# Performance work log

Hardware: AMD Instinct MI355X
Metric: run time of the kernel (lower is better)

Reference implementation:

```python
import jax, jax.numpy as jnp
import numpy as np

H0, H1, NHID, BATCH = 256, 256, 512, 2048

def setup_inputs() -> dict:
    key = jax.random.key(0)
    k1, k2, k3, k4, k5 = jax.random.split(key, 5)
    initrange = 0.1
    inputs = jax.random.normal(k1, (BATCH, NHID), dtype=jnp.float32)
    labels = jax.random.randint(k2, (BATCH,), 0, H1, dtype=jnp.int32)
    parent_labels = jax.random.randint(k3, (BATCH,), 0, H0, dtype=jnp.int32)
    layer_top_W = jax.random.uniform(k4, (NHID, H0), jnp.float32, -initrange, initrange)
    layer_top_b = jnp.zeros((H0,), jnp.float32)
    layer_bottom_W = jax.random.uniform(k5, (H0, NHID, H1), jnp.float32, -initrange, initrange)
    layer_bottom_b = jnp.zeros((H0, H1), jnp.float32)
    return {"inputs": inputs, "labels": labels, "parent_labels": parent_labels,
            "layer_top_W": layer_top_W, "layer_top_b": layer_top_b,
            "layer_bottom_W": layer_bottom_W, "layer_bottom_b": layer_bottom_b}

def reference(inputs, labels, parent_labels, layer_top_W, layer_top_b,
              layer_bottom_W, layer_bottom_b):
    batch = inputs.shape[0]
    # top-level softmax over coarse classes: [B, H0]
    top_probs = jax.nn.softmax(inputs @ layer_top_W + layer_top_b, axis=1)
    # per-sample gather of expert weight slice [B, NHID, H1] then bmm
    Wb = layer_bottom_W[parent_labels]            # [B, NHID, H1]
    bb = layer_bottom_b[parent_labels]            # [B, H1]
    bottom_logits = jnp.einsum('bd,bdk->bk', inputs, Wb) + bb
    bottom_probs = jax.nn.softmax(bottom_logits, axis=1)
    ar = jnp.arange(batch)
    target_probs = top_probs[ar, parent_labels] * bottom_probs[ar, labels]
    return target_probs
```

## Files before the change

kernel.cpp:

```cpp
#include <hip/hip_runtime.h>

constexpr int BATCH = 2048;
constexpr int NHID  = 512;
constexpr int H0    = 256;
constexpr int H1    = 256;
constexpr int SMAX  = 32;
constexpr int KS    = NHID / 4;

__global__ __launch_bounds__(512, 2) void hs_ksplit(
    const float* __restrict__ x,
    const int*   __restrict__ labels,
    const int*   __restrict__ parents,
    const float* __restrict__ topW,
    const float* __restrict__ topb,
    const float* __restrict__ botW,
    const float* __restrict__ botb,
    float*       __restrict__ out)
{
    const int p  = blockIdx.x;
    const int t  = threadIdx.x;
    const int g  = t >> 6;
    const int l  = t & 63;
    const int kw = g & 3;
    const bool bot = (g < 4);

    __shared__ int list[BATCH];
    __shared__ int wcnt[8];
    __shared__ __align__(16) float  xs[SMAX][NHID];
    __shared__ __align__(16) float4 redB[3][4][64];
    __shared__ __align__(16) float4 redT[3][4][64];
    __shared__ float psm[2][SMAX];

    int running = 0;
    for (int c = 0; c < BATCH; c += 512) {
        const bool match = (parents[c + t] == p);
        const unsigned long long mask = __ballot(match);
        if (l == 0) wcnt[g] = __popcll(mask);
        __syncthreads();
        int off = running;
        #pragma unroll
        for (int w = 0; w < 8; ++w) {
            const int cw = wcnt[w];
            if (w < g) off += cw;
            running += cw;
        }
        if (match)
            list[off + __popcll(mask & ((1ull << l) - 1ull))] = c + t;
        __syncthreads();
    }
    const int n = running;
    if (n == 0) return;

    const float* Wbase = bot
        ? botW + (size_t)p * NHID * H1 + (size_t)kw * KS * H1
        : topW + (size_t)kw * KS * H0;
    const float4 b4 = bot ? *(const float4*)(botb + (size_t)p * H1 + 4 * l)
                          : *(const float4*)(topb + 4 * l);
    const int koff = kw * KS;

    for (int base = 0; base < n; base += SMAX) {
        const int rem  = min(SMAX, n - base);
        const int ngrp = (rem + 7) >> 3;
        const int nrow = 8 * ngrp;

        for (int s0 = 0; s0 < nrow; s0 += 4) {
            const int row = s0 + (t >> 7);
            const int idx = list[base + min(row, rem - 1)];
            ((float4*)xs[row])[t & 127] =
                ((const float4*)(x + (size_t)idx * NHID))[t & 127];
        }
        __syncthreads();

        float4 acc[4][8];
        #pragma unroll
        for (int gr = 0; gr < 4; ++gr)
            #pragma unroll
            for (int s = 0; s < 8; ++s)
                acc[gr][s] = make_float4(0.f, 0.f, 0.f, 0.f);

        const float* Wp = Wbase + 4 * l;
        float4 ring[8];
        #pragma unroll
        for (int i = 0; i < 8; ++i)
            ring[i] = *(const float4*)(Wp + (size_t)i * 256);

        for (int d = 0; d < KS; d += 8) {
            #pragma unroll
            for (int h = 0; h < 2; ++h) {
                const int dd = d + 4 * h;
                const float4 w0 = ring[4 * h + 0], w1 = ring[4 * h + 1];
                const float4 w2 = ring[4 * h + 2], w3 = ring[4 * h + 3];
                if (dd + 8 < KS) {
                    #pragma unroll
                    for (int i = 0; i < 4; ++i)
                        ring[4 * h + i] =
                            *(const float4*)(Wp + (size_t)(dd + 8 + i) * 256);
                }
                #pragma unroll
                for (int gr = 0; gr < 4; ++gr) {
                    if (gr < ngrp) {
                        #pragma unroll
                        for (int s = 0; s < 8; ++s) {
                            const float4 xv =
                                *(const float4*)&xs[8 * gr + s][koff + dd];
                            float4 a = acc[gr][s];
                            a.x = fmaf(xv.x, w0.x, a.x); a.y = fmaf(xv.x, w0.y, a.y);
                            a.z = fmaf(xv.x, w0.z, a.z); a.w = fmaf(xv.x, w0.w, a.w);
                            a.x = fmaf(xv.y, w1.x, a.x); a.y = fmaf(xv.y, w1.y, a.y);
                            a.z = fmaf(xv.y, w1.z, a.z); a.w = fmaf(xv.y, w1.w, a.w);
                            a.x = fmaf(xv.z, w2.x, a.x); a.y = fmaf(xv.z, w2.y, a.y);
                            a.z = fmaf(xv.z, w2.z, a.z); a.w = fmaf(xv.z, w2.w, a.w);
                            a.x = fmaf(xv.w, w3.x, a.x); a.y = fmaf(xv.w, w3.y, a.y);
                            a.z = fmaf(xv.w, w3.z, a.z); a.w = fmaf(xv.w, w3.w, a.w);
                            acc[gr][s] = a;
                        }
                    }
                }
            }
        }

        float4 (*red)[4][64] = bot ? redB : redT;
        #pragma unroll
        for (int gr = 0; gr < 4; ++gr) {
            if (gr < ngrp) {
                #pragma unroll
                for (int hf = 0; hf < 2; ++hf) {
                    if (kw != 0) {
                        #pragma unroll
                        for (int si = 0; si < 4; ++si)
                            red[kw - 1][si][l] = acc[gr][4 * hf + si];
                    }
                    __syncthreads();
                    if (kw == 0) {
                        #pragma unroll
                        for (int si = 0; si < 4; ++si) {
                            const int s = 8 * gr + 4 * hf + si;
                            const float4 r0 = red[0][si][l];
                            const float4 r1 = red[1][si][l];
                            const float4 r2 = red[2][si][l];
                            float4 v = acc[gr][4 * hf + si];
                            v.x += r0.x + r1.x + r2.x + b4.x;
                            v.y += r0.y + r1.y + r2.y + b4.y;
                            v.z += r0.z + r1.z + r2.z + b4.z;
                            v.w += r0.w + r1.w + r2.w + b4.w;

                            float m = fmaxf(fmaxf(v.x, v.y), fmaxf(v.z, v.w));
                            #pragma unroll
                            for (int off = 32; off > 0; off >>= 1)
                                m = fmaxf(m, __shfl_xor(m, off, 64));

                            const float ex = expf(v.x - m), ey = expf(v.y - m);
                            const float ez = expf(v.z - m), ew = expf(v.w - m);
                            float sum = (ex + ey) + (ez + ew);
                            #pragma unroll
                            for (int off = 32; off > 0; off >>= 1)
                                sum += __shfl_xor(sum, off, 64);

                            const int tgt =
                                bot ? labels[list[base + min(s, rem - 1)]] : p;
                            const int k = tgt & 3;
                            const float ev = (k == 0) ? ex : (k == 1) ? ey
                                           : (k == 2) ? ez : ew;
                            if (l == (tgt >> 2))
                                psm[bot ? 1 : 0][s] = ev / sum;
                        }
                    }
                    __syncthreads();
                }
            }
        }

        if (t < rem) {
            const int idx = list[base + t];
            out[idx] = psm[0][t] * psm[1][t];
        }
        __syncthreads();
    }
}

extern "C" void kernel_launch(void* const* d_in, const int* in_sizes, int n_in,
                              void* d_out, int out_size, void* d_ws, size_t ws_size,
                              hipStream_t stream) {
    const float* x       = (const float*)d_in[0];
    const int*   labels  = (const int*)  d_in[1];
    const int*   parents = (const int*)  d_in[2];
    const float* topW    = (const float*)d_in[3];
    const float* topb    = (const float*)d_in[4];
    const float* botW    = (const float*)d_in[5];
    const float* botb    = (const float*)d_in[6];
    float*       out     = (float*)d_out;

    hs_ksplit<<<H0, 512, 0, stream>>>(x, labels, parents,
                                      topW, topb, botW, botb, out);
}
```

Before: 228.7 us.

## Stream weights through LDS ring with async global_load_lds, split samples across waves

Replaces the per-wave K-split with register-prefetched weight rows by a 4-deep LDS ring buffer, filled with async global_load_lds instructions and synchronised by explicit vmcnt waits and barriers. Each wave now covers the full K range for a subset of sample slots, which removes the cross-wave partial-sum reduction and its many barriers. SMAX is halved to 16, and all waves share each weight tile from LDS. In exchange, a block-wide barrier is added on every K step, and processing only 16 samples per pass may reload the full weight matrix more often when an expert has more than 16 samples.

```diff
diff --git a/kernel.cpp b/kernel.cpp
--- a/kernel.cpp
+++ b/kernel.cpp
@@ -1,13 +1,26 @@
 #include <hip/hip_runtime.h>
+#include <stdint.h>
 
-constexpr int BATCH = 2048;
-constexpr int NHID  = 512;
-constexpr int H0    = 256;
-constexpr int H1    = 256;
-constexpr int SMAX  = 32;
-constexpr int KS    = NHID / 4;
+constexpr int BATCH  = 2048;
+constexpr int NHID   = 512;
+constexpr int H0     = 256;
+constexpr int H1     = 256;
+constexpr int SMAX   = 16;
+constexpr int KSTEP  = 8;
+constexpr int NSTEPS = NHID / KSTEP;
+constexpr int NBUF   = 4;
 
-__global__ __launch_bounds__(512, 2) void hs_ksplit(
+__device__ __forceinline__ void gload_lds16(const float* gsrc, float* ldst) {
+    __builtin_amdgcn_global_load_lds(
+        (const __attribute__((address_space(1))) void*)gsrc,
+        (__attribute__((address_space(3))) void*)ldst, 16, 0, 0);
+}
+
+#define FMA4(xc, wr) \
+    a.x = fmaf((xc), (wr).x, a.x); a.y = fmaf((xc), (wr).y, a.y); \
+    a.z = fmaf((xc), (wr).z, a.z); a.w = fmaf((xc), (wr).w, a.w)
+
+__global__ __launch_bounds__(512) void hs_v5(
     const float* __restrict__ x,
     const int*   __restrict__ labels,
     const int*   __restrict__ parents,
@@ -21,14 +34,14 @@
     const int t  = threadIdx.x;
     const int g  = t >> 6;
     const int l  = t & 63;
-    const int kw = g & 3;
+    const int ws = g & 3;
     const bool bot = (g < 4);
 
     __shared__ int list[BATCH];
     __shared__ int wcnt[8];
-    __shared__ __align__(16) float  xs[SMAX][NHID];
-    __shared__ __align__(16) float4 redB[3][4][64];
-    __shared__ __align__(16) float4 redT[3][4][64];
+    __shared__ __align__(16) float xs[SMAX][NHID];
+    __shared__ __align__(16) float Wb[NBUF][KSTEP][H1];
+    __shared__ __align__(16) float Wt[NBUF][KSTEP][H0];
     __shared__ float psm[2][SMAX];
 
     int running = 0;
@@ -51,17 +64,23 @@
     const int n = running;
     if (n == 0) return;
 
-    const float* Wbase = bot
-        ? botW + (size_t)p * NHID * H1 + (size_t)kw * KS * H1
-        : topW + (size_t)kw * KS * H0;
+    const float* botWp = botW + (size_t)p * NHID * H1;
     const float4 b4 = bot ? *(const float4*)(botb + (size_t)p * H1 + 4 * l)
                           : *(const float4*)(topb + 4 * l);
-    const int koff = kw * KS;
+
+    #define STAGE(kk) do {                                                   \
+        const int _b = (kk) & (NBUF - 1);                                    \
+        gload_lds16(botWp + (size_t)(kk) * (KSTEP * H1) + g * 256 + l * 4,   \
+                    &Wb[_b][0][0] + g * 256);                                \
+        gload_lds16(topW  + (size_t)(kk) * (KSTEP * H0) + g * 256 + l * 4,   \
+                    &Wt[_b][0][0] + g * 256);                                \
+    } while (0)
 
     for (int base = 0; base < n; base += SMAX) {
         const int rem  = min(SMAX, n - base);
-        const int ngrp = (rem + 7) >> 3;
-        const int nrow = 8 * ngrp;
+        const bool hi  = (rem > 8);
+        const int nsl  = hi ? 4 : 2;
+        const int nrow = hi ? 16 : 8;
 
         for (int s0 = 0; s0 < nrow; s0 += 4) {
             const int row = s0 + (t >> 7);
@@ -71,104 +90,75 @@
         }
         __syncthreads();
 
-        float4 acc[4][8];
+        float4 acc[4];
         #pragma unroll
-        for (int gr = 0; gr < 4; ++gr)
+        for (int i = 0; i < 4; ++i) acc[i] = make_float4(0.f, 0.f, 0.f, 0.f);
+
+        STAGE(0); STAGE(1); STAGE(2);
+
+        for (int k = 0; k < NSTEPS; ++k) {
+            if (k <= NSTEPS - 3)
+                asm volatile("s_waitcnt vmcnt(4)" ::: "memory");
+            else if (k == NSTEPS - 2)
+                asm volatile("s_waitcnt vmcnt(2)" ::: "memory");
+            else
+                asm volatile("s_waitcnt vmcnt(0)" ::: "memory");
+            __builtin_amdgcn_s_barrier();
+            asm volatile("" ::: "memory");
+
+            if (k + 3 < NSTEPS) STAGE(k + 3);
+
+            const int buf = k & (NBUF - 1);
+            const float* Wl = bot ? &Wb[0][0][0] : &Wt[0][0][0];
+            float4 wrow[KSTEP];
             #pragma unroll
-            for (int s = 0; s < 8; ++s)
-                acc[gr][s] = make_float4(0.f, 0.f, 0.f, 0.f);
+            for (int r = 0; r < KSTEP; ++r)
+                wrow[r] = *(const float4*)(Wl + (buf * KSTEP + r) * 256 + 4 * l);
 
-        const float* Wp = Wbase + 4 * l;
-        float4 ring[8];
-        #pragma unroll
-        for (int i = 0; i < 8; ++i)
-            ring[i] = *(const float4*)(Wp + (size_t)i * 256);
-
-        for (int d = 0; d < KS; d += 8) {
+            float4 xa[4], xb[4];
             #pragma unroll
-            for (int h = 0; h < 2; ++h) {
-                const int dd = d + 4 * h;
-                const float4 w0 = ring[4 * h + 0], w1 = ring[4 * h + 1];
-                const float4 w2 = ring[4 * h + 2], w3 = ring[4 * h + 3];
-                if (dd + 8 < KS) {
-                    #pragma unroll
-                    for (int i = 0; i < 4; ++i)
-                        ring[4 * h + i] =
-                            *(const float4*)(Wp + (size_t)(dd + 8 + i) * 256);
-                }
-                #pragma unroll
-                for (int gr = 0; gr < 4; ++gr) {
-                    if (gr < ngrp) {
-                        #pragma unroll
-                        for (int s = 0; s < 8; ++s) {
-                            const float4 xv =
-                                *(const float4*)&xs[8 * gr + s][koff + dd];
-                            float4 a = acc[gr][s];
-                            a.x = fmaf(xv.x, w0.x, a.x); a.y = fmaf(xv.x, w0.y, a.y);
-                            a.z = fmaf(xv.x, w0.z, a.z); a.w = fmaf(xv.x, w0.w, a.w);
-                            a.x = fmaf(xv.y, w1.x, a.x); a.y = fmaf(xv.y, w1.y, a.y);
-                            a.z = fmaf(xv.y, w1.z, a.z); a.w = fmaf(xv.y, w1.w, a.w);
-                            a.x = fmaf(xv.z, w2.x, a.x); a.y = fmaf(xv.z, w2.y, a.y);
-                            a.z = fmaf(xv.z, w2.z, a.z); a.w = fmaf(xv.z, w2.w, a.w);
-                            a.x = fmaf(xv.w, w3.x, a.x); a.y = fmaf(xv.w, w3.y, a.y);
-                            a.z = fmaf(xv.w, w3.z, a.z); a.w = fmaf(xv.w, w3.w, a.w);
-                            acc[gr][s] = a;
-                        }
-                    }
-                }
+            for (int i = 0; i < 4; ++i) if (i < nsl) {
+                const int slot = nsl * ws + i;
+                xa[i] = *(const float4*)&xs[slot][KSTEP * k];
+                xb[i] = *(const float4*)&xs[slot][KSTEP * k + 4];
+            }
+            #pragma unroll
+            for (int i = 0; i < 4; ++i) if (i < nsl) {
+                float4 a = acc[i];
+                FMA4(xa[i].x, wrow[0]); FMA4(xa[i].y, wrow[1]);
+                FMA4(xa[i].z, wrow[2]); FMA4(xa[i].w, wrow[3]);
+                FMA4(xb[i].x, wrow[4]); FMA4(xb[i].y, wrow[5]);
+                FMA4(xb[i].z, wrow[6]); FMA4(xb[i].w, wrow[7]);
+                acc[i] = a;
             }
         }
 
-        float4 (*red)[4][64] = bot ? redB : redT;
         #pragma unroll
-        for (int gr = 0; gr < 4; ++gr) {
-            if (gr < ngrp) {
-                #pragma unroll
-                for (int hf = 0; hf < 2; ++hf) {
-                    if (kw != 0) {
-                        #pragma unroll
-                        for (int si = 0; si < 4; ++si)
-                            red[kw - 1][si][l] = acc[gr][4 * hf + si];
-                    }
-                    __syncthreads();
-                    if (kw == 0) {
-                        #pragma unroll
-                        for (int si = 0; si < 4; ++si) {
-                            const int s = 8 * gr + 4 * hf + si;
-                            const float4 r0 = red[0][si][l];
-                            const float4 r1 = red[1][si][l];
-                            const float4 r2 = red[2][si][l];
-                            float4 v = acc[gr][4 * hf + si];
-                            v.x += r0.x + r1.x + r2.x + b4.x;
-                            v.y += r0.y + r1.y + r2.y + b4.y;
-                            v.z += r0.z + r1.z + r2.z + b4.z;
-                            v.w += r0.w + r1.w + r2.w + b4.w;
+        for (int i = 0; i < 4; ++i) if (i < nsl) {
+            const int slot = nsl * ws + i;
+            float4 v = acc[i];
+            v.x += b4.x; v.y += b4.y; v.z += b4.z; v.w += b4.w;
 
-                            float m = fmaxf(fmaxf(v.x, v.y), fmaxf(v.z, v.w));
-                            #pragma unroll
-                            for (int off = 32; off > 0; off >>= 1)
-                                m = fmaxf(m, __shfl_xor(m, off, 64));
+            float m = fmaxf(fmaxf(v.x, v.y), fmaxf(v.z, v.w));
+            #pragma unroll
+            for (int off = 32; off > 0; off >>= 1)
+                m = fmaxf(m, __shfl_xor(m, off, 64));
 
-                            const float ex = expf(v.x - m), ey = expf(v.y - m);
-                            const float ez = expf(v.z - m), ew = expf(v.w - m);
-                            float sum = (ex + ey) + (ez + ew);
-                            #pragma unroll
-                            for (int off = 32; off > 0; off >>= 1)
-                                sum += __shfl_xor(sum, off, 64);
+            const float ex = expf(v.x - m), ey = expf(v.y - m);
+            const float ez = expf(v.z - m), ew = expf(v.w - m);
+            float sum = (ex + ey) + (ez + ew);
+            #pragma unroll
+            for (int off = 32; off > 0; off >>= 1)
+                sum += __shfl_xor(sum, off, 64);
 
-                            const int tgt =
-                                bot ? labels[list[base + min(s, rem - 1)]] : p;
-                            const int k = tgt & 3;
-                            const float ev = (k == 0) ? ex : (k == 1) ? ey
-                                           : (k == 2) ? ez : ew;
-                            if (l == (tgt >> 2))
-                                psm[bot ? 1 : 0][s] = ev / sum;
-                        }
-                    }
-                    __syncthreads();
-                }
-            }
+            const int tgt = bot ? labels[list[base + min(slot, rem - 1)]] : p;
+            const int kc  = tgt & 3;
+            const float ev = (kc == 0) ? ex : (kc == 1) ? ey
+                           : (kc == 2) ? ez : ew;
+            if (l == (tgt >> 2))
+                psm[bot ? 1 : 0][slot] = ev / sum;
         }
+        __syncthreads();
 
         if (t < rem) {
             const int idx = list[base + t];
@@ -176,6 +166,7 @@
         }
         __syncthreads();
     }
+    #undef STAGE
 }
 
 extern "C" void kernel_launch(void* const* d_in, const int* in_sizes, int n_in,
@@ -190,6 +181,6 @@
     const float* botb    = (const float*)d_in[6];
     float*       out     = (float*)d_out;
 
-    hs_ksplit<<<H0, 512, 0, stream>>>(x, labels, parents,
-                                      topW, topb, botW, botb, out);
+    hs_v5<<<H0, 512, 0, stream>>>(x, labels, parents,
+                                  topW, topb, botW, botb, out);
 }
```

Measured after the change: 285.2 us. 24.7% more time.
